# Performance work log

Hardware: AMD Instinct MI355X
Metric: run time of the kernel (lower is better)

Reference implementation:

```python
import jax, jax.numpy as jnp
import numpy as np

F_IN1 = 256
F_IN2 = 256
F_OUT = 64
ALPHA = 0.2  # LeakyReLU negative slope
NEG_BIG = -9e15


def setup_inputs() -> dict:
    key = jax.random.key(0)
    k1, k2, k3, k4, k5, k6 = jax.random.split(key, 6)
    N1, N2 = 8192, 8192
    h1 = jax.random.normal(k1, (N1, F_IN1), dtype=jnp.float32)
    h2 = jax.random.normal(k2, (N2, F_IN2), dtype=jnp.float32)
    adj = jax.random.normal(k3, (N1, N2), dtype=jnp.float32)  # >0 ~ half the entries = edges
    # Xavier-uniform-ish parameter init (gain folded into scale)
    def xavier(k, shape, gain=1.414):
        fan_in, fan_out = shape[0], shape[1]
        bound = gain * np.sqrt(6.0 / (fan_in + fan_out))
        return jax.random.uniform(k, shape, jnp.float32, -bound, bound)
    W1 = xavier(k4, (F_IN1, F_OUT))
    W2 = xavier(k5, (F_IN2, F_OUT))
    a = xavier(k6, (2 * F_OUT, 1))
    return {"h1": h1, "h2": h2, "adj": adj, "W1": W1, "W2": W2, "a": a}


def reference(h1, h2, adj, W1, W2, a):
    Wh1 = h1 @ W1                       # [N1, F_OUT]
    Wh2 = h2 @ W2                       # [N2, F_OUT]
    s1 = Wh1 @ a[:F_OUT]                # [N1, 1]
    s2 = Wh2 @ a[F_OUT:]                # [N2, 1]
    e = jax.nn.leaky_relu(s1 + s2.T, negative_slope=ALPHA)  # [N1, N2]
    attention = jnp.where(adj > 0, e, NEG_BIG)
    attention1 = jax.nn.softmax(attention, axis=1)  # row softmax
    attention2 = jax.nn.softmax(attention, axis=0)  # col softmax
    h_prime2 = attention1.T @ Wh1       # [N2, F_OUT]
    h_prime1 = attention2 @ Wh2         # [N1, F_OUT]
    return (jax.nn.elu(h_prime1), jax.nn.elu(h_prime2))
```

## Files before the change

kernel.cpp:

```cpp
#include <hip/hip_runtime.h>
#include <hip/hip_bf16.h>


#define N 8192
#define FIN 256
#define FOUT 64

typedef float f32x4 __attribute__((ext_vector_type(4)));
typedef short s16x8 __attribute__((ext_vector_type(8)));
typedef unsigned short u16;

__device__ __forceinline__ u16 f2bf(float x) {
  unsigned u = __builtin_bit_cast(unsigned, x);
  return (u16)((u + 0x7FFFu + ((u >> 16) & 1u)) >> 16);
}

__device__ __forceinline__ float eval_e(float adjv, float s1v, float s2v) {
  float x = s1v + s2v;
  float lr = fmaxf(x, 0.2f * x);
  float e = __expf(lr);
  return adjv > 0.0f ? e : 0.0f;
}

__global__ __launch_bounds__(256) void k_prep(
    const float* __restrict__ h1, const float* __restrict__ h2,
    const float* __restrict__ W1, const float* __restrict__ W2,
    const float* __restrict__ a,
    float* __restrict__ Wh1T, float* __restrict__ Wh2T,
    float* __restrict__ s1, float* __restrict__ s2) {
  __shared__ float hbuf[16][FIN];
  const int t = threadIdx.x;
  const int r0 = blockIdx.x * 16;
  const int f = t & 63, q = t >> 6;
  const int lrow = t >> 4, lc0 = (t & 15) * 16;
  for (int mat = 0; mat < 2; ++mat) {
    const float* h = mat ? h2 : h1;
    const float* W = mat ? W2 : W1;
    float* WhT = mat ? Wh2T : Wh1T;
    float* so = mat ? s2 : s1;
    const float av = a[mat * FOUT + f];
    __syncthreads();
    const float* src = h + (size_t)(r0 + lrow) * FIN + lc0;
#pragma unroll
    for (int u = 0; u < 4; ++u)
      *(f32x4*)&hbuf[lrow][lc0 + u * 4] = *(const f32x4*)(src + u * 4);
    __syncthreads();
    float acc[4] = {0.f, 0.f, 0.f, 0.f};
    for (int k = 0; k < FIN; ++k) {
      float wv = W[k * FOUT + f];
#pragma unroll
      for (int rg = 0; rg < 4; ++rg)
        acc[rg] = fmaf(hbuf[rg * 4 + q][k], wv, acc[rg]);
    }
#pragma unroll
    for (int rg = 0; rg < 4; ++rg) {
      int r = r0 + rg * 4 + q;
      WhT[(size_t)f * N + r] = acc[rg];
      float sp = acc[rg] * av;
#pragma unroll
      for (int m = 1; m < 64; m <<= 1) sp += __shfl_xor(sp, m, 64);
      if (f == 0) so[r] = sp;
    }
  }
}

__global__ __launch_bounds__(256) void k_stats(
    const float* __restrict__ adj, const float* __restrict__ s1,
    const float* __restrict__ s2, float* __restrict__ Z1,
    float* __restrict__ Z2) {
  const int t = threadIdx.x;
  const int c0 = blockIdx.x * 1024 + t * 4;
  const int r0 = blockIdx.y * 32;
  const int wv = t >> 6, lane = t & 63;
  __shared__ float rowpart[4][32];
  const f32x4 s2v = *(const f32x4*)(s2 + c0);
  float ca0 = 0.f, ca1 = 0.f, ca2 = 0.f, ca3 = 0.f;
  for (int rb = 0; rb < 32; rb += 8) {
    f32x4 v[8];
#pragma unroll
    for (int u = 0; u < 8; ++u)
      v[u] = *(const f32x4*)(adj + (size_t)(r0 + rb + u) * N + c0);
#pragma unroll
    for (int u = 0; u < 8; ++u) {
      float s1v = s1[r0 + rb + u];
      float e0 = eval_e(v[u].x, s1v, s2v.x);
      float e1 = eval_e(v[u].y, s1v, s2v.y);
      float e2 = eval_e(v[u].z, s1v, s2v.z);
      float e3 = eval_e(v[u].w, s1v, s2v.w);
      ca0 += e0; ca1 += e1; ca2 += e2; ca3 += e3;
      float rs = (e0 + e1) + (e2 + e3);
#pragma unroll
      for (int m = 1; m < 64; m <<= 1) rs += __shfl_xor(rs, m, 64);
      if (lane == 0) rowpart[wv][rb + u] = rs;
    }
  }
  __syncthreads();
  if (t < 32) {
    float s = rowpart[0][t] + rowpart[1][t] + rowpart[2][t] + rowpart[3][t];
    atomicAdd(&Z1[r0 + t], s);
  }
  atomicAdd(&Z2[c0 + 0], ca0);
  atomicAdd(&Z2[c0 + 1], ca1);
  atomicAdd(&Z2[c0 + 2], ca2);
  atomicAdd(&Z2[c0 + 3], ca3);
}

__global__ __launch_bounds__(256) void k_buildv(
    const float* __restrict__ Wh1T, const float* __restrict__ Wh2T,
    const float* __restrict__ Z1, const float* __restrict__ Z2,
    u16* __restrict__ V1T, u16* __restrict__ V2T) {
  const int mat = blockIdx.y;
  const float* WhT = mat ? Wh2T : Wh1T;
  const float* Z = mat ? Z2 : Z1;
  u16* VT = mat ? V2T : V1T;
  const int idx = (blockIdx.x * 256 + threadIdx.x) * 4;
  const int i = idx & (N - 1);
  f32x4 wh = *(const f32x4*)(WhT + idx);
  f32x4 z = *(const f32x4*)(Z + i);
  unsigned lo = (unsigned)f2bf(wh.x / z.x) | ((unsigned)f2bf(wh.y / z.y) << 16);
  unsigned hi = (unsigned)f2bf(wh.z / z.z) | ((unsigned)f2bf(wh.w / z.w) << 16);
  uint2 uv; uv.x = lo; uv.y = hi;
  *(uint2*)(VT + idx) = uv;
}

#define BI 128
#define BJ 64
#define JC 512

__device__ __forceinline__ int eswz(int il, int jl) {
  return (il * BJ + jl) ^ ((il & 7) << 3);
}

__global__ __launch_bounds__(256) void k_main(
    const float* __restrict__ adj, const float* __restrict__ s1g,
    const float* __restrict__ s2g, const u16* __restrict__ V1T,
    const u16* __restrict__ V2T, float* __restrict__ hp1,
    float* __restrict__ hp2) {
  __shared__ u16 Etile[BI * BJ];
  __shared__ float s1s[BI];
  const int t = threadIdx.x;
  const int w = t >> 6, lane = t & 63;
  const int l15 = lane & 15, l4 = lane >> 4;
  const int i0 = blockIdx.y * BI;
  const int j0 = blockIdx.x * JC;
  if (t < BI) s1s[t] = s1g[i0 + t];
  f32x4 acc1[2][4];
#pragma unroll
  for (int mt = 0; mt < 2; ++mt)
#pragma unroll
    for (int nt = 0; nt < 4; ++nt) acc1[mt][nt] = f32x4{0.f, 0.f, 0.f, 0.f};
  __syncthreads();

  const int cq = t & 15, rr = t >> 4;
  for (int js = 0; js < JC / BJ; ++js) {
    const int j0s = j0 + js * BJ;
    {
      const int jj = j0s + cq * 4;
      const f32x4 s2v = *(const f32x4*)(s2g + jj);
      f32x4 av[8];
#pragma unroll
      for (int p = 0; p < 8; ++p) {
        const int il = p * 16 + rr;
        av[p] = *(const f32x4*)(adj + (size_t)(i0 + il) * N + jj);
      }
#pragma unroll
      for (int p = 0; p < 8; ++p) {
        const int il = p * 16 + rr;
        const float s1v = s1s[il];
        u16 b0 = f2bf(eval_e(av[p].x, s1v, s2v.x));
        u16 b1 = f2bf(eval_e(av[p].y, s1v, s2v.y));
        u16 b2 = f2bf(eval_e(av[p].z, s1v, s2v.z));
        u16 b3 = f2bf(eval_e(av[p].w, s1v, s2v.w));
        uint2 val;
        val.x = (unsigned)b0 | ((unsigned)b1 << 16);
        val.y = (unsigned)b2 | ((unsigned)b3 << 16);
        *(uint2*)&Etile[eswz(il, cq * 4)] = val;
      }
    }
    __syncthreads();
#pragma unroll
    for (int kk = 0; kk < 2; ++kk) {
      s16x8 bfr[4];
#pragma unroll
      for (int nt = 0; nt < 4; ++nt) {
        const int fr = nt * 16 + l15;
        const int jj = j0s + kk * 32 + l4 * 8;
        bfr[nt] = *(const s16x8*)(V2T + (size_t)fr * N + jj);
      }
#pragma unroll
      for (int mt = 0; mt < 2; ++mt) {
        const int il = w * 32 + mt * 16 + l15;
        const int jl = kk * 32 + l4 * 8;
        s16x8 aE = *(const s16x8*)&Etile[eswz(il, jl)];
#pragma unroll
        for (int nt = 0; nt < 4; ++nt)
          acc1[mt][nt] = __builtin_amdgcn_mfma_f32_16x16x32_bf16(
              aE, bfr[nt], acc1[mt][nt], 0, 0, 0);
      }
    }
    {
      const int jj2 = j0s + w * 16 + l15;
      const float s2v = s2g[jj2];
      f32x4 acc2[4];
#pragma unroll
      for (int nt = 0; nt < 4; ++nt) acc2[nt] = f32x4{0.f, 0.f, 0.f, 0.f};
#pragma unroll
      for (int kk = 0; kk < 4; ++kk) {
        float avv[8];
#pragma unroll
        for (int e = 0; e < 8; ++e) {
          const int il = kk * 32 + l4 * 8 + e;
          avv[e] = adj[(size_t)(i0 + il) * N + jj2];
        }
        s16x8 aET;
#pragma unroll
        for (int e = 0; e < 8; ++e) {
          const int il = kk * 32 + l4 * 8 + e;
          aET[e] = (short)f2bf(eval_e(avv[e], s1s[il], s2v));
        }
        s16x8 bfr[4];
#pragma unroll
        for (int nt = 0; nt < 4; ++nt) {
          const int fr = nt * 16 + l15;
          const int ii = i0 + kk * 32 + l4 * 8;
          bfr[nt] = *(const s16x8*)(V1T + (size_t)fr * N + ii);
        }
#pragma unroll
        for (int nt = 0; nt < 4; ++nt)
          acc2[nt] = __builtin_amdgcn_mfma_f32_16x16x32_bf16(
              aET, bfr[nt], acc2[nt], 0, 0, 0);
      }
#pragma unroll
      for (int nt = 0; nt < 4; ++nt)
#pragma unroll
        for (int r = 0; r < 4; ++r) {
          const int jr = j0s + w * 16 + l4 * 4 + r;
          const int fc = nt * 16 + l15;
          atomicAdd(&hp2[(size_t)jr * FOUT + fc], acc2[nt][r]);
        }
    }
    __syncthreads();
  }
#pragma unroll
  for (int mt = 0; mt < 2; ++mt)
#pragma unroll
    for (int nt = 0; nt < 4; ++nt)
#pragma unroll
      for (int r = 0; r < 4; ++r) {
        const int ir = i0 + w * 32 + mt * 16 + l4 * 4 + r;
        const int fc = nt * 16 + l15;
        atomicAdd(&hp1[(size_t)ir * FOUT + fc], acc1[mt][nt][r]);
      }
}

__global__ __launch_bounds__(256) void k_final(const float* __restrict__ hp,
                                               float* __restrict__ out) {
  const int idx = (blockIdx.x * 256 + threadIdx.x) * 4;
  f32x4 v = *(const f32x4*)(hp + idx);
  f32x4 o;
  o.x = v.x > 0.f ? v.x : expm1f(v.x);
  o.y = v.y > 0.f ? v.y : expm1f(v.y);
  o.z = v.z > 0.f ? v.z : expm1f(v.z);
  o.w = v.w > 0.f ? v.w : expm1f(v.w);
  *(f32x4*)(out + idx) = o;
}

extern "C" void kernel_launch(void* const* d_in, const int* in_sizes, int n_in,
                              void* d_out, int out_size, void* d_ws,
                              size_t ws_size, hipStream_t stream) {
  const float* h1 = (const float*)d_in[0];
  const float* h2 = (const float*)d_in[1];
  const float* adj = (const float*)d_in[2];
  const float* W1 = (const float*)d_in[3];
  const float* W2 = (const float*)d_in[4];
  const float* a = (const float*)d_in[5];

  float* ws = (float*)d_ws;
  float* s1 = ws + 0;
  float* s2 = ws + 8192;
  float* Z1 = ws + 16384;
  float* Z2 = ws + 24576;
  float* Wh1T = ws + 32768;
  float* Wh2T = ws + 557056;
  float* hp1 = ws + 1081344;
  float* hp2 = ws + 1605632;
  u16* V1T = (u16*)(ws + 2129920);
  u16* V2T = V1T + 524288;

  hipMemsetAsync(Z1, 0, 2 * 8192 * sizeof(float), stream);
  hipMemsetAsync(hp1, 0, 2 * (size_t)N * FOUT * sizeof(float), stream);

  k_prep<<<512, 256, 0, stream>>>(h1, h2, W1, W2, a, Wh1T, Wh2T, s1, s2);
  k_stats<<<dim3(8, 256), 256, 0, stream>>>(adj, s1, s2, Z1, Z2);
  k_buildv<<<dim3(512, 2), 256, 0, stream>>>(Wh1T, Wh2T, Z1, Z2, V1T, V2T);
  k_main<<<dim3(N / JC, N / BI), 256, 0, stream>>>(adj, s1, s2, V1T, V2T, hp1, hp2);
  k_final<<<1024, 256, 0, stream>>>(hp1, (float*)d_out);
}
```

Before: 284.6 us.

## Reuse computed attention tile via transposed LDS copy instead of reloading adj

The second (column) MFMA pass used to reload adj from global memory with strided scalar loads and recompute exp/leaky-relu for every element. Now the first pass computes each 4x4 patch once, writes both a row-major and a transposed swizzled bf16 tile into LDS, and the column pass reads its operands straight from LDS. This halves adj global traffic and drops the duplicate exp work, at the cost of doubled LDS usage and extra shared stores. Launch bounds also request four blocks per SIMD occupancy.

```diff
diff --git a/kernel.cpp b/kernel.cpp
--- a/kernel.cpp
+++ b/kernel.cpp
@@ -130,13 +130,17 @@
 __device__ __forceinline__ int eswz(int il, int jl) {
   return (il * BJ + jl) ^ ((il & 7) << 3);
 }
-
-__global__ __launch_bounds__(256) void k_main(
+__device__ __forceinline__ int etswz(int jl, int il) {
+  return (jl * BI + il) ^ ((jl & 0x1E) << 2);
+}
+
+__global__ __launch_bounds__(256, 4) void k_main(
     const float* __restrict__ adj, const float* __restrict__ s1g,
     const float* __restrict__ s2g, const u16* __restrict__ V1T,
     const u16* __restrict__ V2T, float* __restrict__ hp1,
     float* __restrict__ hp2) {
   __shared__ u16 Etile[BI * BJ];
+  __shared__ u16 EtileT[BJ * BI];
   __shared__ float s1s[BI];
   const int t = threadIdx.x;
   const int w = t >> 6, lane = t & 63;
@@ -157,24 +161,36 @@
     {
       const int jj = j0s + cq * 4;
       const f32x4 s2v = *(const f32x4*)(s2g + jj);
-      f32x4 av[8];
-#pragma unroll
-      for (int p = 0; p < 8; ++p) {
-        const int il = p * 16 + rr;
-        av[p] = *(const f32x4*)(adj + (size_t)(i0 + il) * N + jj);
-      }
-#pragma unroll
-      for (int p = 0; p < 8; ++p) {
-        const int il = p * 16 + rr;
-        const float s1v = s1s[il];
-        u16 b0 = f2bf(eval_e(av[p].x, s1v, s2v.x));
-        u16 b1 = f2bf(eval_e(av[p].y, s1v, s2v.y));
-        u16 b2 = f2bf(eval_e(av[p].z, s1v, s2v.z));
-        u16 b3 = f2bf(eval_e(av[p].w, s1v, s2v.w));
-        uint2 val;
-        val.x = (unsigned)b0 | ((unsigned)b1 << 16);
-        val.y = (unsigned)b2 | ((unsigned)b3 << 16);
-        *(uint2*)&Etile[eswz(il, cq * 4)] = val;
+#pragma unroll
+      for (int p = 0; p < 2; ++p) {
+        const int il0 = (rr + p * 16) * 4;
+        f32x4 av[4];
+#pragma unroll
+        for (int r = 0; r < 4; ++r)
+          av[r] = *(const f32x4*)(adj + (size_t)(i0 + il0 + r) * N + jj);
+        u16 eb[4][4];
+#pragma unroll
+        for (int r = 0; r < 4; ++r) {
+          const float s1v = s1s[il0 + r];
+          eb[r][0] = f2bf(eval_e(av[r].x, s1v, s2v.x));
+          eb[r][1] = f2bf(eval_e(av[r].y, s1v, s2v.y));
+          eb[r][2] = f2bf(eval_e(av[r].z, s1v, s2v.z));
+          eb[r][3] = f2bf(eval_e(av[r].w, s1v, s2v.w));
+        }
+#pragma unroll
+        for (int r = 0; r < 4; ++r) {
+          uint2 val;
+          val.x = (unsigned)eb[r][0] | ((unsigned)eb[r][1] << 16);
+          val.y = (unsigned)eb[r][2] | ((unsigned)eb[r][3] << 16);
+          *(uint2*)&Etile[eswz(il0 + r, cq * 4)] = val;
+        }
+#pragma unroll
+        for (int c = 0; c < 4; ++c) {
+          uint2 val;
+          val.x = (unsigned)eb[0][c] | ((unsigned)eb[1][c] << 16);
+          val.y = (unsigned)eb[2][c] | ((unsigned)eb[3][c] << 16);
+          *(uint2*)&EtileT[etswz(cq * 4 + c, il0)] = val;
+        }
       }
     }
     __syncthreads();
@@ -199,25 +215,13 @@
       }
     }
     {
-      const int jj2 = j0s + w * 16 + l15;
-      const float s2v = s2g[jj2];
+      const int jl2 = w * 16 + l15;
       f32x4 acc2[4];
 #pragma unroll
       for (int nt = 0; nt < 4; ++nt) acc2[nt] = f32x4{0.f, 0.f, 0.f, 0.f};
 #pragma unroll
       for (int kk = 0; kk < 4; ++kk) {
-        float avv[8];
-#pragma unroll
-        for (int e = 0; e < 8; ++e) {
-          const int il = kk * 32 + l4 * 8 + e;
-          avv[e] = adj[(size_t)(i0 + il) * N + jj2];
-        }
-        s16x8 aET;
-#pragma unroll
-        for (int e = 0; e < 8; ++e) {
-          const int il = kk * 32 + l4 * 8 + e;
-          aET[e] = (short)f2bf(eval_e(avv[e], s1s[il], s2v));
-        }
+        s16x8 aET = *(const s16x8*)&EtileT[etswz(jl2, kk * 32 + l4 * 8)];
         s16x8 bfr[4];
 #pragma unroll
         for (int nt = 0; nt < 4; ++nt) {
```

New measurement: 330.9 us. 16.3% more time.

## Pack adjacency into bitmask in stats pass and split main into hp1/hp2 kernels

Applied to the files above, without the earlier changes.

The stats kernel now also writes a 1-bit-per-entry adjacency mask, so the two aggregation kernels read 8 MB of bits instead of re-reading the 256 MB fp32 adjacency matrix up to twice. The fused main kernel is split into separate row- and column-direction MFMA kernels that rebuild attention values from the mask and s1/s2 in registers, with no LDS tile or block barriers. It also uses truncating bf16 conversion and a single final ELU kernel covering both outputs. The cost is extra mask writes and recomputed exponentials in both kernels.

```diff
diff --git a/kernel.cpp b/kernel.cpp
--- a/kernel.cpp
+++ b/kernel.cpp
@@ -9,17 +9,17 @@
 typedef float f32x4 __attribute__((ext_vector_type(4)));
 typedef short s16x8 __attribute__((ext_vector_type(8)));
 typedef unsigned short u16;
+typedef unsigned long long u64;
 
 __device__ __forceinline__ u16 f2bf(float x) {
   unsigned u = __builtin_bit_cast(unsigned, x);
   return (u16)((u + 0x7FFFu + ((u >> 16) & 1u)) >> 16);
 }
-
-__device__ __forceinline__ float eval_e(float adjv, float s1v, float s2v) {
-  float x = s1v + s2v;
-  float lr = fmaxf(x, 0.2f * x);
-  float e = __expf(lr);
-  return adjv > 0.0f ? e : 0.0f;
+__device__ __forceinline__ u16 f2bf_t(float x) {
+  return (u16)(__builtin_bit_cast(unsigned, x) >> 16);
+}
+__device__ __forceinline__ float lrexp(float x) {
+  return __expf(fmaxf(x, 0.2f * x));
 }
 
 __global__ __launch_bounds__(256) void k_prep(
@@ -64,45 +64,70 @@
   }
 }
 
-__global__ __launch_bounds__(256) void k_stats(
+__global__ __launch_bounds__(256) void k_statsmask(
     const float* __restrict__ adj, const float* __restrict__ s1,
     const float* __restrict__ s2, float* __restrict__ Z1,
-    float* __restrict__ Z2) {
+    float* __restrict__ Z2, u16* __restrict__ mask) {
   const int t = threadIdx.x;
-  const int c0 = blockIdx.x * 1024 + t * 4;
+  const int c0 = blockIdx.x * 4096 + t * 16;
   const int r0 = blockIdx.y * 32;
   const int wv = t >> 6, lane = t & 63;
   __shared__ float rowpart[4][32];
-  const f32x4 s2v = *(const f32x4*)(s2 + c0);
-  float ca0 = 0.f, ca1 = 0.f, ca2 = 0.f, ca3 = 0.f;
-  for (int rb = 0; rb < 32; rb += 8) {
-    f32x4 v[8];
-#pragma unroll
-    for (int u = 0; u < 8; ++u)
-      v[u] = *(const f32x4*)(adj + (size_t)(r0 + rb + u) * N + c0);
-#pragma unroll
-    for (int u = 0; u < 8; ++u) {
-      float s1v = s1[r0 + rb + u];
-      float e0 = eval_e(v[u].x, s1v, s2v.x);
-      float e1 = eval_e(v[u].y, s1v, s2v.y);
-      float e2 = eval_e(v[u].z, s1v, s2v.z);
-      float e3 = eval_e(v[u].w, s1v, s2v.w);
-      ca0 += e0; ca1 += e1; ca2 += e2; ca3 += e3;
-      float rs = (e0 + e1) + (e2 + e3);
-#pragma unroll
-      for (int m = 1; m < 64; m <<= 1) rs += __shfl_xor(rs, m, 64);
-      if (lane == 0) rowpart[wv][rb + u] = rs;
-    }
+  float s2v[16];
+#pragma unroll
+  for (int e = 0; e < 16; e += 4)
+    *(f32x4*)&s2v[e] = *(const f32x4*)(s2 + c0 + e);
+  f32x4 ca[4];
+#pragma unroll
+  for (int q = 0; q < 4; ++q) ca[q] = f32x4{0.f, 0.f, 0.f, 0.f};
+
+  f32x4 va[4], vb[4];
+#pragma unroll
+  for (int q = 0; q < 4; ++q)
+    va[q] = *(const f32x4*)(adj + (size_t)r0 * N + c0 + q * 4);
+
+  auto loadrow = [&](int r, f32x4 (&v)[4]) {
+#pragma unroll
+    for (int q = 0; q < 4; ++q)
+      v[q] = *(const f32x4*)(adj + (size_t)(r0 + r) * N + c0 + q * 4);
+  };
+  auto proc = [&](int r, f32x4 (&v)[4]) {
+    const float s1v = s1[r0 + r];
+    unsigned m = 0;
+    float rs = 0.f;
+#pragma unroll
+    for (int q = 0; q < 4; ++q)
+#pragma unroll
+      for (int c = 0; c < 4; ++c) {
+        const int e = q * 4 + c;
+        float ev = lrexp(s1v + s2v[e]);
+        const bool on = v[q][c] > 0.f;
+        ev = on ? ev : 0.f;
+        m |= on ? (1u << e) : 0u;
+        ca[q][c] += ev;
+        rs += ev;
+      }
+    mask[(size_t)(r0 + r) * 512 + (c0 >> 4)] = (u16)m;
+#pragma unroll
+    for (int sh = 1; sh < 64; sh <<= 1) rs += __shfl_xor(rs, sh, 64);
+    if (lane == 0) rowpart[wv][r] = rs;
+  };
+
+  for (int r = 0; r < 32; r += 2) {
+    loadrow(r + 1, vb);
+    proc(r, va);
+    if (r + 2 < 32) loadrow(r + 2, va);
+    proc(r + 1, vb);
   }
   __syncthreads();
   if (t < 32) {
     float s = rowpart[0][t] + rowpart[1][t] + rowpart[2][t] + rowpart[3][t];
     atomicAdd(&Z1[r0 + t], s);
   }
-  atomicAdd(&Z2[c0 + 0], ca0);
-  atomicAdd(&Z2[c0 + 1], ca1);
-  atomicAdd(&Z2[c0 + 2], ca2);
-  atomicAdd(&Z2[c0 + 3], ca3);
+#pragma unroll
+  for (int q = 0; q < 4; ++q)
+#pragma unroll
+    for (int c = 0; c < 4; ++c) atomicAdd(&Z2[c0 + q * 4 + c], ca[q][c]);
 }
 
 __global__ __launch_bounds__(256) void k_buildv(
@@ -123,146 +148,173 @@
   *(uint2*)(VT + idx) = uv;
 }
 
-#define BI 128
-#define BJ 64
-#define JC 512
-
-__device__ __forceinline__ int eswz(int il, int jl) {
-  return (il * BJ + jl) ^ ((il & 7) << 3);
-}
-
-__global__ __launch_bounds__(256) void k_main(
-    const float* __restrict__ adj, const float* __restrict__ s1g,
+__global__ __launch_bounds__(256) void k_hp1(
+    const u16* __restrict__ maskp, const float* __restrict__ s1g,
+    const float* __restrict__ s2g, const u16* __restrict__ V2T,
+    float* __restrict__ hp1) {
+  const int t = threadIdx.x, w = t >> 6, lane = t & 63;
+  const int l15 = lane & 15, l4 = lane >> 4;
+  const int sh0 = l4 * 8;
+  const int i0 = blockIdx.x * 128 + w * 32;
+  const int jbase = blockIdx.y * 512;
+  const u64* mrow0 = (const u64*)maskp + (size_t)(i0 + l15) * 128;
+  const u64* mrow1 = mrow0 + 16 * 128;
+  const float s1v0 = s1g[i0 + l15];
+  const float s1v1 = s1g[i0 + 16 + l15];
+  f32x4 acc[2][4];
+#pragma unroll
+  for (int mt = 0; mt < 2; ++mt)
+#pragma unroll
+    for (int nt = 0; nt < 4; ++nt) acc[mt][nt] = f32x4{0.f, 0.f, 0.f, 0.f};
+
+#pragma unroll 2
+  for (int js = 0; js < 8; ++js) {
+    const int j0s = jbase + js * 64;
+    const u64 m0 = mrow0[j0s >> 6];
+    const u64 m1 = mrow1[j0s >> 6];
+    f32x4 s2q[4];
+#pragma unroll
+    for (int kk = 0; kk < 2; ++kk)
+#pragma unroll
+      for (int h = 0; h < 2; ++h)
+        s2q[kk * 2 + h] = *(const f32x4*)(s2g + j0s + kk * 32 + sh0 + h * 4);
+    s16x8 bf[2][4];
+#pragma unroll
+    for (int kk = 0; kk < 2; ++kk)
+#pragma unroll
+      for (int nt = 0; nt < 4; ++nt)
+        bf[kk][nt] = *(const s16x8*)(V2T + (size_t)(nt * 16 + l15) * N + j0s +
+                                     kk * 32 + sh0);
+    s16x8 afr[2][2];
+#pragma unroll
+    for (int kk = 0; kk < 2; ++kk) {
+      const unsigned b0 = (unsigned)(kk ? (m0 >> 32) : m0);
+      const unsigned b1 = (unsigned)(kk ? (m1 >> 32) : m1);
+#pragma unroll
+      for (int e = 0; e < 8; ++e) {
+        const float s2e = s2q[kk * 2 + (e >> 2)][e & 3];
+        float e0 = lrexp(s1v0 + s2e);
+        float e1 = lrexp(s1v1 + s2e);
+        e0 = ((b0 >> (sh0 + e)) & 1u) ? e0 : 0.f;
+        e1 = ((b1 >> (sh0 + e)) & 1u) ? e1 : 0.f;
+        afr[0][kk][e] = (short)f2bf_t(e0);
+        afr[1][kk][e] = (short)f2bf_t(e1);
+      }
+    }
+#pragma unroll
+    for (int nt = 0; nt < 4; ++nt) {
+      acc[0][nt] = __builtin_amdgcn_mfma_f32_16x16x32_bf16(afr[0][0], bf[0][nt],
+                                                           acc[0][nt], 0, 0, 0);
+      acc[0][nt] = __builtin_amdgcn_mfma_f32_16x16x32_bf16(afr[0][1], bf[1][nt],
+                                                           acc[0][nt], 0, 0, 0);
+      acc[1][nt] = __builtin_amdgcn_mfma_f32_16x16x32_bf16(afr[1][0], bf[0][nt],
+                                                           acc[1][nt], 0, 0, 0);
+      acc[1][nt] = __builtin_amdgcn_mfma_f32_16x16x32_bf16(afr[1][1], bf[1][nt],
+                                                           acc[1][nt], 0, 0, 0);
+    }
+  }
+#pragma unroll
+  for (int mt = 0; mt < 2; ++mt)
+#pragma unroll
+    for (int nt = 0; nt < 4; ++nt)
+#pragma unroll
+      for (int r = 0; r < 4; ++r)
+        atomicAdd(&hp1[(size_t)(i0 + mt * 16 + l4 * 4 + r) * 64 + nt * 16 + l15],
+                  acc[mt][nt][r]);
+}
+
+__global__ __launch_bounds__(256) void k_hp2(
+    const u16* __restrict__ maskp, const float* __restrict__ s1g,
     const float* __restrict__ s2g, const u16* __restrict__ V1T,
-    const u16* __restrict__ V2T, float* __restrict__ hp1,
     float* __restrict__ hp2) {
-  __shared__ u16 Etile[BI * BJ];
-  __shared__ float s1s[BI];
-  const int t = threadIdx.x;
-  const int w = t >> 6, lane = t & 63;
+  const int t = threadIdx.x, w = t >> 6, lane = t & 63;
   const int l15 = lane & 15, l4 = lane >> 4;
-  const int i0 = blockIdx.y * BI;
-  const int j0 = blockIdx.x * JC;
-  if (t < BI) s1s[t] = s1g[i0 + t];
-  f32x4 acc1[2][4];
+  const int sh0 = l4 * 8;
+  const int j0w = blockIdx.x * 128 + w * 32;
+  const int ibase = blockIdx.y * 512;
+  const float s2vA = s2g[j0w + l15];
+  const float s2vB = s2g[j0w + 16 + l15];
+  const unsigned* mask32 = (const unsigned*)maskp;
+  const int wsel = j0w >> 5;
+  f32x4 acc[2][4];
 #pragma unroll
   for (int mt = 0; mt < 2; ++mt)
 #pragma unroll
-    for (int nt = 0; nt < 4; ++nt) acc1[mt][nt] = f32x4{0.f, 0.f, 0.f, 0.f};
-  __syncthreads();
-
-  const int cq = t & 15, rr = t >> 4;
-  for (int js = 0; js < JC / BJ; ++js) {
-    const int j0s = j0 + js * BJ;
-    {
-      const int jj = j0s + cq * 4;
-      const f32x4 s2v = *(const f32x4*)(s2g + jj);
-      f32x4 av[8];
-#pragma unroll
-      for (int p = 0; p < 8; ++p) {
-        const int il = p * 16 + rr;
-        av[p] = *(const f32x4*)(adj + (size_t)(i0 + il) * N + jj);
+    for (int nt = 0; nt < 4; ++nt) acc[mt][nt] = f32x4{0.f, 0.f, 0.f, 0.f};
+
+#pragma unroll 2
+  for (int tile = 0; tile < 8; ++tile) {
+    const int it0 = ibase + tile * 64;
+    f32x4 s1q[4];
+#pragma unroll
+    for (int kk = 0; kk < 2; ++kk)
+#pragma unroll
+      for (int h = 0; h < 2; ++h)
+        s1q[kk * 2 + h] = *(const f32x4*)(s1g + it0 + kk * 32 + sh0 + h * 4);
+    unsigned mw[2][8];
+#pragma unroll
+    for (int kk = 0; kk < 2; ++kk)
+#pragma unroll
+      for (int e = 0; e < 8; ++e)
+        mw[kk][e] = mask32[(size_t)(it0 + kk * 32 + sh0 + e) * 256 + wsel];
+    s16x8 bf[2][4];
+#pragma unroll
+    for (int kk = 0; kk < 2; ++kk)
+#pragma unroll
+      for (int nt = 0; nt < 4; ++nt)
+        bf[kk][nt] = *(const s16x8*)(V1T + (size_t)(nt * 16 + l15) * N + it0 +
+                                     kk * 32 + sh0);
+    s16x8 aA[2], aB[2];
+#pragma unroll
+    for (int kk = 0; kk < 2; ++kk)
+#pragma unroll
+      for (int e = 0; e < 8; ++e) {
+        const float s1v = s1q[kk * 2 + (e >> 2)][e & 3];
+        float eA = lrexp(s1v + s2vA);
+        float eB = lrexp(s1v + s2vB);
+        const unsigned mwv = mw[kk][e];
+        eA = ((mwv >> l15) & 1u) ? eA : 0.f;
+        eB = ((mwv >> (16 + l15)) & 1u) ? eB : 0.f;
+        aA[kk][e] = (short)f2bf_t(eA);
+        aB[kk][e] = (short)f2bf_t(eB);
       }
 #pragma unroll
-      for (int p = 0; p < 8; ++p) {
-        const int il = p * 16 + rr;
-        const float s1v = s1s[il];
-        u16 b0 = f2bf(eval_e(av[p].x, s1v, s2v.x));
-        u16 b1 = f2bf(eval_e(av[p].y, s1v, s2v.y));
-        u16 b2 = f2bf(eval_e(av[p].z, s1v, s2v.z));
-        u16 b3 = f2bf(eval_e(av[p].w, s1v, s2v.w));
-        uint2 val;
-        val.x = (unsigned)b0 | ((unsigned)b1 << 16);
-        val.y = (unsigned)b2 | ((unsigned)b3 << 16);
-        *(uint2*)&Etile[eswz(il, cq * 4)] = val;
-      }
-    }
-    __syncthreads();
-#pragma unroll
-    for (int kk = 0; kk < 2; ++kk) {
-      s16x8 bfr[4];
-#pragma unroll
-      for (int nt = 0; nt < 4; ++nt) {
-        const int fr = nt * 16 + l15;
-        const int jj = j0s + kk * 32 + l4 * 8;
-        bfr[nt] = *(const s16x8*)(V2T + (size_t)fr * N + jj);
-      }
-#pragma unroll
-      for (int mt = 0; mt < 2; ++mt) {
-        const int il = w * 32 + mt * 16 + l15;
-        const int jl = kk * 32 + l4 * 8;
-        s16x8 aE = *(const s16x8*)&Etile[eswz(il, jl)];
-#pragma unroll
-        for (int nt = 0; nt < 4; ++nt)
-          acc1[mt][nt] = __builtin_amdgcn_mfma_f32_16x16x32_bf16(
-              aE, bfr[nt], acc1[mt][nt], 0, 0, 0);
-      }
-    }
-    {
-      const int jj2 = j0s + w * 16 + l15;
-      const float s2v = s2g[jj2];
-      f32x4 acc2[4];
-#pragma unroll
-      for (int nt = 0; nt < 4; ++nt) acc2[nt] = f32x4{0.f, 0.f, 0.f, 0.f};
-#pragma unroll
-      for (int kk = 0; kk < 4; ++kk) {
-        float avv[8];
-#pragma unroll
-        for (int e = 0; e < 8; ++e) {
-          const int il = kk * 32 + l4 * 8 + e;
-          avv[e] = adj[(size_t)(i0 + il) * N + jj2];
-        }
-        s16x8 aET;
-#pragma unroll
-        for (int e = 0; e < 8; ++e) {
-          const int il = kk * 32 + l4 * 8 + e;
-          aET[e] = (short)f2bf(eval_e(avv[e], s1s[il], s2v));
-        }
-        s16x8 bfr[4];
-#pragma unroll
-        for (int nt = 0; nt < 4; ++nt) {
-          const int fr = nt * 16 + l15;
-          const int ii = i0 + kk * 32 + l4 * 8;
-          bfr[nt] = *(const s16x8*)(V1T + (size_t)fr * N + ii);
-        }
-#pragma unroll
-        for (int nt = 0; nt < 4; ++nt)
-          acc2[nt] = __builtin_amdgcn_mfma_f32_16x16x32_bf16(
-              aET, bfr[nt], acc2[nt], 0, 0, 0);
-      }
-#pragma unroll
-      for (int nt = 0; nt < 4; ++nt)
-#pragma unroll
-        for (int r = 0; r < 4; ++r) {
-          const int jr = j0s + w * 16 + l4 * 4 + r;
-          const int fc = nt * 16 + l15;
-          atomicAdd(&hp2[(size_t)jr * FOUT + fc], acc2[nt][r]);
-        }
-    }
-    __syncthreads();
+    for (int nt = 0; nt < 4; ++nt) {
+      acc[0][nt] = __builtin_amdgcn_mfma_f32_16x16x32_bf16(aA[0], bf[0][nt],
+                                                           acc[0][nt], 0, 0, 0);
+      acc[0][nt] = __builtin_amdgcn_mfma_f32_16x16x32_bf16(aA[1], bf[1][nt],
+                                                           acc[0][nt], 0, 0, 0);
+      acc[1][nt] = __builtin_amdgcn_mfma_f32_16x16x32_bf16(aB[0], bf[0][nt],
+                                                           acc[1][nt], 0, 0, 0);
+      acc[1][nt] = __builtin_amdgcn_mfma_f32_16x16x32_bf16(aB[1], bf[1][nt],
+                                                           acc[1][nt], 0, 0, 0);
+    }
   }
 #pragma unroll
   for (int mt = 0; mt < 2; ++mt)
 #pragma unroll
     for (int nt = 0; nt < 4; ++nt)
 #pragma unroll
-      for (int r = 0; r < 4; ++r) {
-        const int ir = i0 + w * 32 + mt * 16 + l4 * 4 + r;
-        const int fc = nt * 16 + l15;
-        atomicAdd(&hp1[(size_t)ir * FOUT + fc], acc1[mt][nt][r]);
-      }
-}
-
-__global__ __launch_bounds__(256) void k_final(const float* __restrict__ hp,
-                                               float* __restrict__ out) {
-  const int idx = (blockIdx.x * 256 + threadIdx.x) * 4;
-  f32x4 v = *(const f32x4*)(hp + idx);
-  f32x4 o;
-  o.x = v.x > 0.f ? v.x : expm1f(v.x);
-  o.y = v.y > 0.f ? v.y : expm1f(v.y);
-  o.z = v.z > 0.f ? v.z : expm1f(v.z);
-  o.w = v.w > 0.f ? v.w : expm1f(v.w);
-  *(f32x4*)(out + idx) = o;
+      for (int r = 0; r < 4; ++r)
+        atomicAdd(
+            &hp2[(size_t)(j0w + mt * 16 + l4 * 4 + r) * 64 + nt * 16 + l15],
+            acc[mt][nt][r]);
+}
+
+__global__ __launch_bounds__(256) void k_red(const float* __restrict__ hp1,
+                                             const float* __restrict__ hp2,
+                                             float* __restrict__ out) {
+  const size_t idx = ((size_t)blockIdx.x * 256 + threadIdx.x) * 4;
+  f32x4 v1 = *(const f32x4*)(hp1 + idx);
+  f32x4 v2 = *(const f32x4*)(hp2 + idx);
+  f32x4 o1, o2;
+#pragma unroll
+  for (int c = 0; c < 4; ++c) {
+    o1[c] = v1[c] > 0.f ? v1[c] : expm1f(v1[c]);
+    o2[c] = v2[c] > 0.f ? v2[c] : expm1f(v2[c]);
+  }
+  *(f32x4*)(out + idx) = o1;
+  *(f32x4*)(out + (size_t)N * FOUT + idx) = o2;
 }
 
 extern "C" void kernel_launch(void* const* d_in, const int* in_sizes, int n_in,
@@ -282,17 +334,19 @@
   float* Z2 = ws + 24576;
   float* Wh1T = ws + 32768;
   float* Wh2T = ws + 557056;
-  float* hp1 = ws + 1081344;
-  float* hp2 = ws + 1605632;
-  u16* V1T = (u16*)(ws + 2129920);
+  u16* V1T = (u16*)(ws + 1081344);
   u16* V2T = V1T + 524288;
+  u16* mask = (u16*)(ws + 1605632);
+  float* hp1 = ws + 3702784;
+  float* hp2 = ws + 4227072;
 
   hipMemsetAsync(Z1, 0, 2 * 8192 * sizeof(float), stream);
   hipMemsetAsync(hp1, 0, 2 * (size_t)N * FOUT * sizeof(float), stream);
 
   k_prep<<<512, 256, 0, stream>>>(h1, h2, W1, W2, a, Wh1T, Wh2T, s1, s2);
-  k_stats<<<dim3(8, 256), 256, 0, stream>>>(adj, s1, s2, Z1, Z2);
+  k_statsmask<<<dim3(2, 256), 256, 0, stream>>>(adj, s1, s2, Z1, Z2, mask);
   k_buildv<<<dim3(512, 2), 256, 0, stream>>>(Wh1T, Wh2T, Z1, Z2, V1T, V2T);
-  k_main<<<dim3(N / JC, N / BI), 256, 0, stream>>>(adj, s1, s2, V1T, V2T, hp1, hp2);
-  k_final<<<1024, 256, 0, stream>>>(hp1, (float*)d_out);
-}
+  k_hp1<<<dim3(64, 16), 256, 0, stream>>>(mask, s1, s2, V2T, hp1);
+  k_hp2<<<dim3(64, 16), 256, 0, stream>>>(mask, s1, s2, V1T, hp2);
+  k_red<<<512, 256, 0, stream>>>(hp1, hp2, (float*)d_out);
+}
```

Result: slower. 355.6 us (+24.9%).
